# Performance work log

Measured on AMD Instinct MI355X. Metric: run time of the kernel, lower is better.

Reference implementation:

```python
import jax, jax.numpy as jnp
import numpy as np

BPTT, BSZ, NTOKEN = 32, 32, 2000
NINP, NHID = 1024, 256


def setup_inputs() -> dict:
    key = jax.random.key(0)
    ks = jax.random.split(key, 8)
    s = 0.1  # matches uniform(-0.1, 0.1) init scale
    return {
        "input": jax.random.normal(ks[0], (BPTT, BSZ, NTOKEN), jnp.float32),
        "b": jax.random.normal(ks[1], (BSZ, NHID), jnp.float32),
        "RBF_w": jax.random.uniform(ks[2], (NINP, NTOKEN), jnp.float32, -s, s),
        "RBF_b": jnp.zeros((NINP,), jnp.float32),
        "emb_w": jax.random.uniform(ks[3], (NHID, NINP), jnp.float32, -s, s),
        "emb_b": jnp.zeros((NHID,), jnp.float32),
        "wfef_w": jax.random.uniform(ks[4], (NHID * NHID, NHID), jnp.float32, -s, s),
        "wfef_b": jnp.zeros((NHID * NHID,), jnp.float32),
        "dec_w": jax.random.uniform(ks[5], (NTOKEN, NHID), jnp.float32, -s, s),
        "dec_b": jnp.zeros((NTOKEN,), jnp.float32),
    }


def reference(input, b, RBF_w, RBF_b, emb_w, emb_b, wfef_w, wfef_b, dec_w, dec_b):
    bptt, bsz, ntoken = input.shape
    nhid = b.shape[1]
    ninp = RBF_w.shape[0]
    rbf_scale = np.float32(np.sqrt(2.0) / np.sqrt(ninp))
    # random Fourier features: cos(RBF(x)) * sqrt(2/ninp)
    encoded = jnp.cos(input @ RBF_w.T + RBF_b) * rbf_scale      # [bptt,bsz,ninp]
    obs = encoded @ emb_w.T + emb_b                              # [bptt,bsz,nhid]

    def step(b_t, obs_t):
        # per-sample transition matrix from current state
        W = (b_t @ wfef_w.T + wfef_b).reshape(bsz, nhid, nhid)   # [bsz,nhid,nhid]
        bn = jnp.einsum('brc,bc->br', W, obs_t)                  # [bsz,nhid]
        bn = bn / jnp.sqrt(jnp.sum(bn * bn, axis=1, keepdims=True))
        out = bn @ dec_w.T + dec_b                               # [bsz,ntoken]
        return bn, out

    b_final, outputs = jax.lax.scan(step, b, obs)                # outputs: [bptt,bsz,ntoken]
    return outputs, b_final
```

## Files before the change

kernel.cpp:

```cpp
#include <hip/hip_runtime.h>
#include <hip/hip_fp16.h>
#include <math.h>

typedef _Float16 half_t;
typedef __attribute__((ext_vector_type(2))) _Float16 f16x2;
typedef __attribute__((ext_vector_type(4))) _Float16 f16x4;
typedef __attribute__((ext_vector_type(8))) _Float16 f16x8;
typedef __attribute__((ext_vector_type(4))) float f32x4;

#define BPTT 32
#define BSZ 32
#define NTOK 2000
#define NTOKP 2048
#define NINP 1024
#define NHID 256
#define TB 1024
#define NH2 65536
#define TCH 8
#define FUSED_LDS 25600
#define FRONT_LDS 24576

__device__ __forceinline__ int swz(int row, int hoff) {
  return (row * 32 + hoff) ^ ((row & 7) << 3);
}

__global__ void cvtAll_k(const float* __restrict__ input, half_t* __restrict__ A1hi,
                         half_t* __restrict__ A1lo, const float* __restrict__ RBF_w,
                         half_t* __restrict__ B1hi, half_t* __restrict__ B1lo,
                         const float* __restrict__ emb_w,
                         const float* __restrict__ wfef_b,
                         const float* __restrict__ dec_w, half_t* __restrict__ B2,
                         half_t* __restrict__ WBh, half_t* __restrict__ B4) {
  int bid = blockIdx.x;
  if (bid < 16384) {
    const float* src;
    half_t *hi, *lo;
    int idx;
    if (bid < 8192) {
      src = input; hi = A1hi; lo = A1lo; idx = bid * 256 + threadIdx.x;
    } else {
      src = RBF_w; hi = B1hi; lo = B1lo; idx = (bid - 8192) * 256 + threadIdx.x;
    }
    int r = idx >> 11, c = idx & 2047;
    float v = (c < NTOK) ? src[(size_t)r * NTOK + c] : 0.f;
    half_t h = (half_t)v;
    hi[idx] = h;
    lo[idx] = (half_t)(v - (float)h);
    return;
  }
  int i = (bid - 16384) * 256 + threadIdx.x;
  if (i < 262144) { B2[i] = (half_t)emb_w[i]; return; }
  i -= 262144;
  if (i < 65536) { WBh[i] = (half_t)wfef_b[i]; return; }
  i -= 65536;
  int r = i >> 8, c = i & 255;
  B4[i] = (half_t)((r < NTOK) ? dec_w[(size_t)r * 256 + c] : 0.f);
}

template <int EP>
__global__ __launch_bounds__(256) void gemm128_k(const half_t* __restrict__ A,
                                                 const half_t* __restrict__ B,
                                                 void* __restrict__ C,
                                                 const float* __restrict__ bias, int K,
                                                 int ldc) {
  __shared__ half_t As[128 * 32];
  __shared__ half_t Bs[128 * 32];
  const int tid = threadIdx.x;
  const int lane = tid & 63, wave = tid >> 6;
  const int wr = wave >> 1, wc = wave & 1;
  const int row0 = blockIdx.x * 128, col0 = blockIdx.y * 128;
  const int srow = tid >> 2, sseg = tid & 3;
  const size_t aoff = (size_t)(row0 + srow) * K + sseg * 8;
  const size_t boff = (size_t)(col0 + srow) * K + sseg * 8;
  const int fr = lane & 15, fq = lane >> 4;

  f32x4 acc[4][4];
#pragma unroll
  for (int m = 0; m < 4; m++)
#pragma unroll
    for (int n = 0; n < 4; n++) acc[m][n] = (f32x4)(0.0f);

  for (int k0 = 0; k0 < K; k0 += 32) {
    f16x8 a0 = *(const f16x8*)(A + aoff + k0);
    f16x8 a1 = *(const f16x8*)(A + aoff + (size_t)64 * K + k0);
    f16x8 b0 = *(const f16x8*)(B + boff + k0);
    f16x8 b1 = *(const f16x8*)(B + boff + (size_t)64 * K + k0);
    __syncthreads();
    *(f16x8*)(As + swz(srow, sseg * 8)) = a0;
    *(f16x8*)(As + swz(srow + 64, sseg * 8)) = a1;
    *(f16x8*)(Bs + swz(srow, sseg * 8)) = b0;
    *(f16x8*)(Bs + swz(srow + 64, sseg * 8)) = b1;
    __syncthreads();
    f16x8 af[4], bf[4];
#pragma unroll
    for (int m = 0; m < 4; m++)
      af[m] = *(const f16x8*)(As + swz(wr * 64 + m * 16 + fr, fq * 8));
#pragma unroll
    for (int n = 0; n < 4; n++)
      bf[n] = *(const f16x8*)(Bs + swz(wc * 64 + n * 16 + fr, fq * 8));
#pragma unroll
    for (int m = 0; m < 4; m++)
#pragma unroll
      for (int n = 0; n < 4; n++)
        acc[m][n] = __builtin_amdgcn_mfma_f32_16x16x32_f16(af[m], bf[n], acc[m][n], 0, 0, 0);
  }

#pragma unroll
  for (int m = 0; m < 4; m++)
#pragma unroll
    for (int n = 0; n < 4; n++)
#pragma unroll
      for (int j = 0; j < 4; j++) {
        int gr = row0 + wr * 64 + m * 16 + fq * 4 + j;
        int gc = col0 + wc * 64 + n * 16 + fr;
        float v = acc[m][n][j];
        if (EP == 1) {
          ((half_t*)C)[(size_t)gr * ldc + gc] = (half_t)(v + bias[gc]);
        } else {
          ((float*)C)[(size_t)gr * ldc + gc] = v;
        }
      }
}

template <int EP>
__device__ __forceinline__ void gemmMC_body(const half_t* __restrict__ A,
                                            const half_t* __restrict__ B,
                                            void* __restrict__ C,
                                            const float* __restrict__ bias, int col0,
                                            int ldc, int nvalid, char* smem) {
  half_t* As = (half_t*)smem;
  half_t* Bs = (half_t*)(smem + 16384);
  const int tid = threadIdx.x;
  const int lane = tid & 63, wave = tid >> 6;
  const int wr = wave >> 2, wc = wave & 3;
  const int srow = tid >> 2, sseg = tid & 3;
  const int fr = lane & 15, fq = lane >> 4;
  const size_t aoff = (size_t)srow * 256 + sseg * 8;
  const size_t boff = (size_t)(col0 + (srow & 127)) * 256 + sseg * 8;

  f32x4 acc[4][2];
#pragma unroll
  for (int m = 0; m < 4; m++)
#pragma unroll
    for (int n = 0; n < 2; n++) acc[m][n] = (f32x4)(0.0f);

  for (int k0 = 0; k0 < 256; k0 += 32) {
    f16x8 a0 = *(const f16x8*)(A + aoff + k0);
    f16x8 b0;
    if (tid < 512) b0 = *(const f16x8*)(B + boff + k0);
    __syncthreads();
    *(f16x8*)(As + swz(srow, sseg * 8)) = a0;
    if (tid < 512) *(f16x8*)(Bs + swz(srow, sseg * 8)) = b0;
    __syncthreads();
    f16x8 af[4], bf[2];
#pragma unroll
    for (int m = 0; m < 4; m++)
      af[m] = *(const f16x8*)(As + swz(wr * 64 + m * 16 + fr, fq * 8));
#pragma unroll
    for (int n = 0; n < 2; n++)
      bf[n] = *(const f16x8*)(Bs + swz(wc * 32 + n * 16 + fr, fq * 8));
#pragma unroll
    for (int m = 0; m < 4; m++)
#pragma unroll
      for (int n = 0; n < 2; n++)
        acc[m][n] = __builtin_amdgcn_mfma_f32_16x16x32_f16(af[m], bf[n], acc[m][n], 0, 0, 0);
  }

#pragma unroll
  for (int m = 0; m < 4; m++)
#pragma unroll
    for (int n = 0; n < 2; n++)
#pragma unroll
      for (int j = 0; j < 4; j++) {
        int gr = wr * 64 + m * 16 + fq * 4 + j;
        int gc = col0 + wc * 32 + n * 16 + fr;
        if (EP == 0) {
          ((half_t*)C)[(size_t)gr * ldc + gc] = (half_t)acc[m][n][j];
        } else {
          if (gc < nvalid)
            ((float*)C)[(size_t)gr * ldc + gc] = acc[m][n][j] + bias[gc];
        }
      }
}

__device__ void scan_body(const half_t* __restrict__ Mc, const float* __restrict__ V,
                          int t0, const float* __restrict__ bin,
                          float* __restrict__ bstate, half_t* __restrict__ BN,
                          float* __restrict__ bfinal, int b, char* smem) {
  float(*Vs)[256] = (float(*)[256])smem;
  float(*partial)[260] = (float(*)[260])(smem + 8192);
  unsigned* bh2 = (unsigned*)(smem + 24832);
  float* red = (float*)(smem + 25344);
  const int tid = threadIdx.x;
  const int hh = tid >> 6, lane = tid & 63;
  const int hpar = lane >> 5, r8 = (lane & 31) * 8;

  if (tid < TCH * 64) {
    int vr = tid >> 6;
    *(f32x4*)&Vs[vr][lane * 4] =
        *(const f32x4*)(V + ((size_t)(t0 + vr) * 32 + b) * 256 + lane * 4);
  }
  if (tid < 128) {
    const float* bs = bin + b * 256 + tid * 2;
    union { f16x2 h; unsigned u; } z;
    z.h[0] = (half_t)bs[0];
    z.h[1] = (half_t)bs[1];
    bh2[tid] = z.u;
  }

  const half_t* mbase = Mc + (size_t)b * NH2 + (size_t)(hh * 16 + hpar) * 256 + r8;
  f16x8 cur[8], nxt[8];
#pragma unroll
  for (int k = 0; k < 8; k++) cur[k] = *(const f16x8*)(mbase + k * 512);
  __syncthreads();

  for (int tt = 0; tt < TCH; tt++) {
    const int tn = (tt < TCH - 1) ? tt + 1 : TCH - 1;
    const half_t* mb2 = mbase + (size_t)tn * 32 * NH2;
#pragma unroll
    for (int k = 0; k < 8; k++) nxt[k] = *(const f16x8*)(mb2 + k * 512);

    uint4 q0 = *(const uint4*)&bh2[hh * 8];
    uint4 q1 = *(const uint4*)&bh2[hh * 8 + 4];
    unsigned bu[8] = {q0.x, q0.y, q0.z, q0.w, q1.x, q1.y, q1.z, q1.w};
    const int sh = hpar * 16;
    half_t hv[8];
#pragma unroll
    for (int k = 0; k < 8; k++)
      hv[k] = __builtin_bit_cast(half_t, (unsigned short)(bu[k] >> sh));

    float a[8] = {0.f, 0.f, 0.f, 0.f, 0.f, 0.f, 0.f, 0.f};
#pragma unroll
    for (int k = 0; k < 8; k++)
#pragma unroll
      for (int j = 0; j < 8; j++) a[j] += (float)cur[k][j] * (float)hv[k];
#pragma unroll
    for (int j = 0; j < 8; j++) a[j] += __shfl_xor(a[j], 32);
    f32x4 st = hpar ? (f32x4){a[4], a[5], a[6], a[7]} : (f32x4){a[0], a[1], a[2], a[3]};
    *(f32x4*)&partial[hh][r8 + hpar * 4] = st;
    __syncthreads();

    float s = 0.f;
    if (tid < 256) {
#pragma unroll
      for (int g = 0; g < 16; g++) s += partial[g][tid];
      s += Vs[tt][tid];
      float sq = s * s;
#pragma unroll
      for (int o = 32; o > 0; o >>= 1) sq += __shfl_xor(sq, o);
      if ((tid & 63) == 0) red[tid >> 6] = sq;
    }
    __syncthreads();
    if (tid < 256) {
      float sumsq = red[0] + red[1] + red[2] + red[3];
      float bnv = s / sqrtf(sumsq);
      float bnv_hi = __shfl_down(bnv, 1);
      if (!(tid & 1)) {
        union { f16x2 h; unsigned u; } z;
        z.h[0] = (half_t)bnv;
        z.h[1] = (half_t)bnv_hi;
        bh2[tid >> 1] = z.u;
        *(unsigned*)(BN + ((size_t)(t0 + tt) * 32 + b) * 256 + tid) = z.u;
      }
      if (tt == TCH - 1) bstate[b * 256 + tid] = bnv;
      if (t0 + tt == BPTT - 1) bfinal[b * 256 + tid] = bnv;
    }
    __syncthreads();
#pragma unroll
    for (int k = 0; k < 8; k++) cur[k] = nxt[k];
  }
}

__global__ __launch_bounds__(1024) void fused_k(
    int scanN, int gemmN, const half_t* __restrict__ Msc,
    const float* __restrict__ Vbuf, int t0, const float* __restrict__ bin,
    float* __restrict__ bstate, half_t* __restrict__ BN,
    float* __restrict__ bfinal, const half_t* __restrict__ Ag,
    const half_t* __restrict__ Bg, half_t* __restrict__ Cg, int decRow0,
    const half_t* __restrict__ BNa, const half_t* __restrict__ B4,
    float* __restrict__ outp, const float* __restrict__ dec_b) {
  extern __shared__ char smem[];
  const int id = blockIdx.x;
  if (id < scanN) {
    scan_body(Msc, Vbuf, t0, bin, bstate, BN, bfinal, id, smem);
  } else if (id < scanN + gemmN) {
    const int g = id - scanN;
    gemmMC_body<0>(Ag, Bg, (void*)Cg, nullptr, g * 128, NH2, 0, smem);
  } else {
    const int d = id - scanN - gemmN;
    const int r0 = decRow0 + (d >> 4) * 256;
    gemmMC_body<3>(BNa + (size_t)r0 * 256, B4, (void*)(outp + (size_t)r0 * NTOK),
                   dec_b, (d & 15) * 128, NTOK, NTOK, smem);
  }
}

__global__ __launch_bounds__(256) void front_k(const half_t* __restrict__ Ahi,
                                               const half_t* __restrict__ Alo,
                                               const half_t* __restrict__ Bhi,
                                               const half_t* __restrict__ Blo,
                                               float* __restrict__ P,
                                               const float* __restrict__ wfef,
                                               half_t* __restrict__ wwt) {
  extern __shared__ char fsm[];
  if (blockIdx.x >= 512) {
    float* tile = (float*)fsm;
    const int p = blockIdx.x - 512;
    const int r = p & 255, cb = (p >> 8) & 3, hb = p >> 10;
    const int tid = threadIdx.x;
    const int l16 = tid & 15, cr = tid >> 4;
#pragma unroll
    for (int i = 0; i < 4; i++) {
      int c = i * 16 + cr;
      int m = ((c >> 3) & 7) << 3;
      f32x4 v = *(const f32x4*)(wfef + ((size_t)(r * 256 + cb * 64 + c)) * 256 +
                                hb * 64 + l16 * 4);
      *(f32x4*)&tile[c * 64 + ((l16 * 4) ^ m)] = v;
    }
    __syncthreads();
    const int cg = tid & 7, hr = tid >> 3;
#pragma unroll
    for (int i = 0; i < 2; i++) {
      int h = i * 32 + hr;
      int hs = h ^ (cg << 3);
      f16x8 o;
#pragma unroll
      for (int j = 0; j < 8; j++) o[j] = (half_t)tile[(cg * 8 + j) * 64 + hs];
      *(f16x8*)(wwt + ((size_t)(hb * 64 + h) * 256 + r) * 256 + cb * 64 + cg * 8) = o;
    }
    return;
  }
  half_t* Ash = (half_t*)fsm;
  half_t* Asl = (half_t*)(fsm + 8192);
  half_t* Bsh = (half_t*)(fsm + 16384);
  half_t* Bsl = (half_t*)(fsm + 20480);
  const int id = blockIdx.x;
  const int kp = id & 3, r2 = id >> 2;
  const int bx = r2 & 7, by = r2 >> 3;
  const int row0 = bx * 128, col0 = by * 64, koff = kp * 512;
  const int tid = threadIdx.x;
  const int lane = tid & 63, wave = tid >> 6;
  const int wr = wave >> 1, wc = wave & 1;
  const int srow = tid >> 2, sseg = tid & 3;
  const size_t aoff = (size_t)(row0 + srow) * NTOKP + koff + sseg * 8;
  const size_t boff = (size_t)(col0 + srow) * NTOKP + koff + sseg * 8;
  const int fr = lane & 15, fq = lane >> 4;

  f32x4 acc[4][2];
#pragma unroll
  for (int m = 0; m < 4; m++)
#pragma unroll
    for (int n = 0; n < 2; n++) acc[m][n] = (f32x4)(0.0f);

  for (int k0 = 0; k0 < 512; k0 += 32) {
    f16x8 ah0 = *(const f16x8*)(Ahi + aoff + k0);
    f16x8 ah1 = *(const f16x8*)(Ahi + aoff + (size_t)64 * NTOKP + k0);
    f16x8 al0 = *(const f16x8*)(Alo + aoff + k0);
    f16x8 al1 = *(const f16x8*)(Alo + aoff + (size_t)64 * NTOKP + k0);
    f16x8 bh0 = *(const f16x8*)(Bhi + boff + k0);
    f16x8 bl0 = *(const f16x8*)(Blo + boff + k0);
    __syncthreads();
    *(f16x8*)(Ash + swz(srow, sseg * 8)) = ah0;
    *(f16x8*)(Ash + swz(srow + 64, sseg * 8)) = ah1;
    *(f16x8*)(Asl + swz(srow, sseg * 8)) = al0;
    *(f16x8*)(Asl + swz(srow + 64, sseg * 8)) = al1;
    *(f16x8*)(Bsh + swz(srow, sseg * 8)) = bh0;
    *(f16x8*)(Bsl + swz(srow, sseg * 8)) = bl0;
    __syncthreads();
    f16x8 afh[4], afl[4], bfh[2], bfl[2];
#pragma unroll
    for (int m = 0; m < 4; m++) {
      afh[m] = *(const f16x8*)(Ash + swz(wr * 64 + m * 16 + fr, fq * 8));
      afl[m] = *(const f16x8*)(Asl + swz(wr * 64 + m * 16 + fr, fq * 8));
    }
#pragma unroll
    for (int n = 0; n < 2; n++) {
      bfh[n] = *(const f16x8*)(Bsh + swz(wc * 32 + n * 16 + fr, fq * 8));
      bfl[n] = *(const f16x8*)(Bsl + swz(wc * 32 + n * 16 + fr, fq * 8));
    }
#pragma unroll
    for (int m = 0; m < 4; m++)
#pragma unroll
      for (int n = 0; n < 2; n++) {
        acc[m][n] = __builtin_amdgcn_mfma_f32_16x16x32_f16(afh[m], bfh[n], acc[m][n], 0, 0, 0);
        acc[m][n] = __builtin_amdgcn_mfma_f32_16x16x32_f16(afl[m], bfh[n], acc[m][n], 0, 0, 0);
        acc[m][n] = __builtin_amdgcn_mfma_f32_16x16x32_f16(afh[m], bfl[n], acc[m][n], 0, 0, 0);
      }
  }

  float* Pk = P + (size_t)kp * (NINP * (size_t)TB);
#pragma unroll
  for (int m = 0; m < 4; m++)
#pragma unroll
    for (int n = 0; n < 2; n++)
#pragma unroll
      for (int j = 0; j < 4; j++) {
        int gr = row0 + wr * 64 + m * 16 + fq * 4 + j;
        int gc = col0 + wc * 32 + n * 16 + fr;
        Pk[(size_t)gr * NINP + gc] = acc[m][n][j];
      }
}

__global__ void rbf_combine_k(const float* __restrict__ P, const float* __restrict__ bias,
                              half_t* __restrict__ C) {
  int idx = blockIdx.x * 256 + threadIdx.x;
  int e0 = idx * 4;
  int col = e0 & (NINP - 1);
  f32x4 s = *(const f32x4*)(P + e0);
  s += *(const f32x4*)(P + (size_t)1 * TB * NINP + e0);
  s += *(const f32x4*)(P + (size_t)2 * TB * NINP + e0);
  s += *(const f32x4*)(P + (size_t)3 * TB * NINP + e0);
  const float RBF_SCALE = 0.04419417382415922f;
  f16x4 o;
#pragma unroll
  for (int j = 0; j < 4; j++) o[j] = (half_t)(cosf(s[j] + bias[col + j]) * RBF_SCALE);
  *(f16x4*)(C + e0) = o;
}


extern "C" void kernel_launch(void* const* d_in, const int* in_sizes, int n_in,
                              void* d_out, int out_size, void* d_ws, size_t ws_size,
                              hipStream_t stream) {
  const float* input = (const float*)d_in[0];
  const float* b0 = (const float*)d_in[1];
  const float* RBF_w = (const float*)d_in[2];
  const float* RBF_b = (const float*)d_in[3];
  const float* emb_w = (const float*)d_in[4];
  const float* emb_b = (const float*)d_in[5];
  const float* wfef_w = (const float*)d_in[6];
  const float* wfef_b = (const float*)d_in[7];
  const float* dec_w = (const float*)d_in[8];
  const float* dec_b = (const float*)d_in[9];

  char* ws = (char*)d_ws;
  size_t off = 0;
  auto alloc = [&](size_t bytes) {
    void* p = ws + off;
    off += (bytes + 255) & ~(size_t)255;
    return p;
  };
  half_t* A1hi = (half_t*)alloc((size_t)TB * NTOKP * 2);
  half_t* A1lo = (half_t*)alloc((size_t)TB * NTOKP * 2);
  half_t* B1hi = (half_t*)alloc((size_t)NINP * NTOKP * 2);
  half_t* B1lo = (half_t*)alloc((size_t)NINP * NTOKP * 2);
  half_t* encA = (half_t*)alloc((size_t)TB * NINP * 2);
  half_t* B2 = (half_t*)alloc((size_t)NHID * NINP * 2);
  half_t* obsA = (half_t*)alloc((size_t)TB * NHID * 2);
  half_t* WBh = (half_t*)alloc((size_t)NHID * NHID * 2);
  half_t* B4 = (half_t*)alloc((size_t)2048 * NHID * 2);
  float* Vbuf = (float*)alloc((size_t)TB * NHID * 4);
  half_t* BN = (half_t*)alloc((size_t)TB * NHID * 2);
  float* bstate = (float*)alloc((size_t)BSZ * NHID * 4);
  half_t* WWT = (half_t*)alloc((size_t)NH2 * NHID * 2);
  half_t* Mmat = (half_t*)alloc((size_t)TB * NH2 * 2);
  if (off > ws_size) return;

  float* Pk = (float*)Mmat;

  float* outp = (float*)d_out;
  float* bfinal = outp + (size_t)TB * NTOK;

  cvtAll_k<<<19712, 256, 0, stream>>>(input, A1hi, A1lo, RBF_w, B1hi, B1lo, emb_w,
                                      wfef_b, dec_w, B2, WBh, B4);
  front_k<<<512 + 4096, 256, FRONT_LDS, stream>>>(A1hi, A1lo, B1hi, B1lo, Pk,
                                                  wfef_w, WWT);
  rbf_combine_k<<<(TB * NINP / 4) / 256, 256, 0, stream>>>(Pk, RBF_b, encA);
  gemm128_k<1><<<dim3(8, 2), 256, 0, stream>>>(encA, B2, obsA, emb_b, NINP, NHID);
  gemm128_k<2><<<dim3(8, 2), 256, 0, stream>>>(obsA, WBh, Vbuf, nullptr, NHID, NHID);

  fused_k<<<512, 1024, FUSED_LDS, stream>>>(
      0, 512, nullptr, Vbuf, 0, b0, bstate, BN, bfinal, obsA, WWT, Mmat, 0, BN, B4,
      outp, dec_b);
  fused_k<<<544, 1024, FUSED_LDS, stream>>>(
      32, 512, Mmat, Vbuf, 0, b0, bstate, BN, bfinal, obsA + (size_t)256 * NHID, WWT,
      Mmat + (size_t)256 * NH2, 0, BN, B4, outp, dec_b);
  fused_k<<<560, 1024, FUSED_LDS, stream>>>(
      32, 512, Mmat + (size_t)256 * NH2, Vbuf, TCH, bstate, bstate, BN, bfinal,
      obsA + (size_t)512 * NHID, WWT, Mmat + (size_t)512 * NH2, 0, BN, B4, outp,
      dec_b);
  fused_k<<<560, 1024, FUSED_LDS, stream>>>(
      32, 512, Mmat + (size_t)512 * NH2, Vbuf, 2 * TCH, bstate, bstate, BN, bfinal,
      obsA + (size_t)768 * NHID, WWT, Mmat + (size_t)768 * NH2, 256, BN, B4, outp,
      dec_b);
  fused_k<<<48, 1024, FUSED_LDS, stream>>>(
      32, 0, Mmat + (size_t)768 * NH2, Vbuf, 3 * TCH, bstate, bstate, BN, bfinal,
      nullptr, nullptr, nullptr, 512, BN, B4, outp, dec_b);
  fused_k<<<16, 1024, FUSED_LDS, stream>>>(
      0, 0, nullptr, Vbuf, 0, bstate, bstate, BN, bfinal, nullptr, nullptr, nullptr,
      768, BN, B4, outp, dec_b);
}
```

Measured before the change: 224.3 us.

## Fold V GEMM into first fused launch and enlarge wfef transpose tiles

Removes the separate gemm128_k<2> launch for V = obs·WBh and computes it inside the first fused_k launch as 8 extra blocks using a new EP==2 epilogue. The wfef transpose blocks in front_k now each handle a full 256-column row slab (1024 blocks instead of 4096) through a 64KB LDS tile with a different swizzle and vectorized reads. The aim is to cut one launch and the per-block overhead of the transpose, in exchange for more LDS per block and lower occupancy in front_k.

```diff
diff --git a/kernel.cpp b/kernel.cpp
--- a/kernel.cpp
+++ b/kernel.cpp
@@ -18,7 +18,7 @@
 #define NH2 65536
 #define TCH 8
 #define FUSED_LDS 25600
-#define FRONT_LDS 24576
+#define FRONT_LDS 65536
 
 __device__ __forceinline__ int swz(int row, int hoff) {
   return (row * 32 + hoff) ^ ((row & 7) << 3);
@@ -113,12 +113,7 @@
       for (int j = 0; j < 4; j++) {
         int gr = row0 + wr * 64 + m * 16 + fq * 4 + j;
         int gc = col0 + wc * 64 + n * 16 + fr;
-        float v = acc[m][n][j];
-        if (EP == 1) {
-          ((half_t*)C)[(size_t)gr * ldc + gc] = (half_t)(v + bias[gc]);
-        } else {
-          ((float*)C)[(size_t)gr * ldc + gc] = v;
-        }
+        ((half_t*)C)[(size_t)gr * ldc + gc] = (half_t)(acc[m][n][j] + bias[gc]);
       }
 }
 
@@ -176,6 +171,8 @@
         int gc = col0 + wc * 32 + n * 16 + fr;
         if (EP == 0) {
           ((half_t*)C)[(size_t)gr * ldc + gc] = (half_t)acc[m][n][j];
+        } else if (EP == 2) {
+          ((float*)C)[(size_t)gr * ldc + gc] = acc[m][n][j];
         } else {
           if (gc < nvalid)
             ((float*)C)[(size_t)gr * ldc + gc] = acc[m][n][j] + bias[gc];
@@ -272,13 +269,15 @@
 }
 
 __global__ __launch_bounds__(1024) void fused_k(
-    int scanN, int gemmN, const half_t* __restrict__ Msc,
+    int scanN, int gemmN, int vN, const half_t* __restrict__ Msc,
     const float* __restrict__ Vbuf, int t0, const float* __restrict__ bin,
     float* __restrict__ bstate, half_t* __restrict__ BN,
     float* __restrict__ bfinal, const half_t* __restrict__ Ag,
-    const half_t* __restrict__ Bg, half_t* __restrict__ Cg, int decRow0,
-    const half_t* __restrict__ BNa, const half_t* __restrict__ B4,
-    float* __restrict__ outp, const float* __restrict__ dec_b) {
+    const half_t* __restrict__ Bg, half_t* __restrict__ Cg,
+    const half_t* __restrict__ obsF, const half_t* __restrict__ WBh,
+    float* __restrict__ Vout, int decRow0, const half_t* __restrict__ BNa,
+    const half_t* __restrict__ B4, float* __restrict__ outp,
+    const float* __restrict__ dec_b) {
   extern __shared__ char smem[];
   const int id = blockIdx.x;
   if (id < scanN) {
@@ -286,8 +285,13 @@
   } else if (id < scanN + gemmN) {
     const int g = id - scanN;
     gemmMC_body<0>(Ag, Bg, (void*)Cg, nullptr, g * 128, NH2, 0, smem);
+  } else if (id < scanN + gemmN + vN) {
+    const int v = id - scanN - gemmN;
+    gemmMC_body<2>(obsF + (size_t)(v >> 1) * 256 * NHID, WBh,
+                   (void*)(Vout + (size_t)(v >> 1) * 256 * 256), nullptr,
+                   (v & 1) * 128, 256, 0, smem);
   } else {
-    const int d = id - scanN - gemmN;
+    const int d = id - scanN - gemmN - vN;
     const int r0 = decRow0 + (d >> 4) * 256;
     gemmMC_body<3>(BNa + (size_t)r0 * 256, B4, (void*)(outp + (size_t)r0 * NTOK),
                    dec_b, (d & 15) * 128, NTOK, NTOK, smem);
@@ -305,27 +309,33 @@
   if (blockIdx.x >= 512) {
     float* tile = (float*)fsm;
     const int p = blockIdx.x - 512;
-    const int r = p & 255, cb = (p >> 8) & 3, hb = p >> 10;
+    const int r = p >> 2, hb = p & 3;
     const int tid = threadIdx.x;
-    const int l16 = tid & 15, cr = tid >> 4;
-#pragma unroll
-    for (int i = 0; i < 4; i++) {
-      int c = i * 16 + cr;
-      int m = ((c >> 3) & 7) << 3;
-      f32x4 v = *(const f32x4*)(wfef + ((size_t)(r * 256 + cb * 64 + c)) * 256 +
-                                hb * 64 + l16 * 4);
-      *(f32x4*)&tile[c * 64 + ((l16 * 4) ^ m)] = v;
-    }
-    __syncthreads();
-    const int cg = tid & 7, hr = tid >> 3;
-#pragma unroll
-    for (int i = 0; i < 2; i++) {
-      int h = i * 32 + hr;
-      int hs = h ^ (cg << 3);
+    const float* src = wfef + (size_t)(r * 256) * 256 + hb * 64;
+#pragma unroll
+    for (int i = 0; i < 16; i++) {
+      int q = i * 256 + tid;
+      int c = q >> 4, qi = q & 15;
+      int f = (qi & 7) << 2;
+      f32x4 v = *(const f32x4*)(src + (size_t)c * 256 + qi * 4);
+#pragma unroll
+      for (int k = 0; k < 4; k++) tile[(qi * 4 + k) * 256 + (c ^ f)] = v[k];
+    }
+    __syncthreads();
+    const int c8 = (tid & 31) * 8, hq = tid >> 5;
+#pragma unroll
+    for (int i = 0; i < 8; i++) {
+      int h = i * 8 + hq;
+      int f = ((h >> 2) & 7) << 2;
+      f32x4 u0 = *(const f32x4*)&tile[h * 256 + (c8 ^ f)];
+      f32x4 u1 = *(const f32x4*)&tile[h * 256 + ((c8 + 4) ^ f)];
       f16x8 o;
 #pragma unroll
-      for (int j = 0; j < 8; j++) o[j] = (half_t)tile[(cg * 8 + j) * 64 + hs];
-      *(f16x8*)(wwt + ((size_t)(hb * 64 + h) * 256 + r) * 256 + cb * 64 + cg * 8) = o;
+      for (int j = 0; j < 4; j++) {
+        o[j] = (half_t)u0[j];
+        o[j + 4] = (half_t)u1[j];
+      }
+      *(f16x8*)(wwt + ((size_t)(hb * 64 + h) * 256 + r) * 256 + c8) = o;
     }
     return;
   }
@@ -461,30 +471,29 @@
 
   cvtAll_k<<<19712, 256, 0, stream>>>(input, A1hi, A1lo, RBF_w, B1hi, B1lo, emb_w,
                                       wfef_b, dec_w, B2, WBh, B4);
-  front_k<<<512 + 4096, 256, FRONT_LDS, stream>>>(A1hi, A1lo, B1hi, B1lo, Pk,
+  front_k<<<512 + 1024, 256, FRONT_LDS, stream>>>(A1hi, A1lo, B1hi, B1lo, Pk,
                                                   wfef_w, WWT);
   rbf_combine_k<<<(TB * NINP / 4) / 256, 256, 0, stream>>>(Pk, RBF_b, encA);
   gemm128_k<1><<<dim3(8, 2), 256, 0, stream>>>(encA, B2, obsA, emb_b, NINP, NHID);
-  gemm128_k<2><<<dim3(8, 2), 256, 0, stream>>>(obsA, WBh, Vbuf, nullptr, NHID, NHID);
-
-  fused_k<<<512, 1024, FUSED_LDS, stream>>>(
-      0, 512, nullptr, Vbuf, 0, b0, bstate, BN, bfinal, obsA, WWT, Mmat, 0, BN, B4,
-      outp, dec_b);
+
+  fused_k<<<520, 1024, FUSED_LDS, stream>>>(
+      0, 512, 8, nullptr, Vbuf, 0, b0, bstate, BN, bfinal, obsA, WWT, Mmat, obsA,
+      WBh, Vbuf, 0, BN, B4, outp, dec_b);
   fused_k<<<544, 1024, FUSED_LDS, stream>>>(
-      32, 512, Mmat, Vbuf, 0, b0, bstate, BN, bfinal, obsA + (size_t)256 * NHID, WWT,
-      Mmat + (size_t)256 * NH2, 0, BN, B4, outp, dec_b);
+      32, 512, 0, Mmat, Vbuf, 0, b0, bstate, BN, bfinal, obsA + (size_t)256 * NHID,
+      WWT, Mmat + (size_t)256 * NH2, obsA, WBh, Vbuf, 0, BN, B4, outp, dec_b);
   fused_k<<<560, 1024, FUSED_LDS, stream>>>(
-      32, 512, Mmat + (size_t)256 * NH2, Vbuf, TCH, bstate, bstate, BN, bfinal,
-      obsA + (size_t)512 * NHID, WWT, Mmat + (size_t)512 * NH2, 0, BN, B4, outp,
-      dec_b);
+      32, 512, 0, Mmat + (size_t)256 * NH2, Vbuf, TCH, bstate, bstate, BN, bfinal,
+      obsA + (size_t)512 * NHID, WWT, Mmat + (size_t)512 * NH2, obsA, WBh, Vbuf, 0,
+      BN, B4, outp, dec_b);
   fused_k<<<560, 1024, FUSED_LDS, stream>>>(
-      32, 512, Mmat + (size_t)512 * NH2, Vbuf, 2 * TCH, bstate, bstate, BN, bfinal,
-      obsA + (size_t)768 * NHID, WWT, Mmat + (size_t)768 * NH2, 256, BN, B4, outp,
-      dec_b);
+      32, 512, 0, Mmat + (size_t)512 * NH2, Vbuf, 2 * TCH, bstate, bstate, BN,
+      bfinal, obsA + (size_t)768 * NHID, WWT, Mmat + (size_t)768 * NH2, obsA, WBh,
+      Vbuf, 256, BN, B4, outp, dec_b);
   fused_k<<<48, 1024, FUSED_LDS, stream>>>(
-      32, 0, Mmat + (size_t)768 * NH2, Vbuf, 3 * TCH, bstate, bstate, BN, bfinal,
-      nullptr, nullptr, nullptr, 512, BN, B4, outp, dec_b);
+      32, 0, 0, Mmat + (size_t)768 * NH2, Vbuf, 3 * TCH, bstate, bstate, BN, bfinal,
+      nullptr, nullptr, nullptr, obsA, WBh, Vbuf, 512, BN, B4, outp, dec_b);
   fused_k<<<16, 1024, FUSED_LDS, stream>>>(
-      0, 0, nullptr, Vbuf, 0, bstate, bstate, BN, bfinal, nullptr, nullptr, nullptr,
-      768, BN, B4, outp, dec_b);
-}
+      0, 0, 0, nullptr, Vbuf, 0, bstate, bstate, BN, bfinal, nullptr, nullptr,
+      nullptr, obsA, WBh, Vbuf, 768, BN, B4, outp, dec_b);
+}
```

After: 229.0 us. 2.1% more time.
